# Kernel tuning notes

Measured on AMD Instinct MI355X. Metric: run time of the kernel, lower is better.

The kernel has to match this reference:

```python
import jax, jax.numpy as jnp
import numpy as np

N = 524288
H = 128
NB = 55  # number of bones


def setup_inputs() -> dict:
    key = jax.random.key(0)
    ks = jax.random.split(key, 8)
    xyz = jax.random.normal(ks[0], (N, 3), dtype=jnp.float32)
    quats = jax.random.normal(ks[1], (N, 4), dtype=jnp.float32)
    # bone transforms: identity-ish affine 4x4 per bone
    tfs = jnp.eye(4, dtype=jnp.float32)[None] + 0.05 * jax.random.normal(ks[2], (NB, 4, 4), dtype=jnp.float32)
    aabb_min = -4.0 * jnp.ones(3, dtype=jnp.float32)
    aabb_max = 4.0 * jnp.ones(3, dtype=jnp.float32)
    W0 = jax.random.normal(ks[3], (3, H), dtype=jnp.float32) / np.sqrt(3.0)
    b0 = jnp.zeros(H, dtype=jnp.float32)
    W1 = jax.random.normal(ks[4], (H, H), dtype=jnp.float32) / np.sqrt(H)
    b1 = jnp.zeros(H, dtype=jnp.float32)
    W2 = jax.random.normal(ks[5], (H, H), dtype=jnp.float32) / np.sqrt(H)
    b2 = jnp.zeros(H, dtype=jnp.float32)
    W3 = jax.random.normal(ks[6], (H, 59), dtype=jnp.float32) / np.sqrt(H)
    b3 = jnp.zeros(59, dtype=jnp.float32)
    return dict(xyz=xyz, quats=quats, tfs=tfs, aabb_min=aabb_min, aabb_max=aabb_max,
                W0=W0, b0=b0, W1=W1, b1=b1, W2=W2, b2=b2, W3=W3, b3=b3)


def hierarchical_softmax(x):
    # x: (N, 59) logits -> (N, 55) probabilities over SMPL-X bones
    s = jax.nn.sigmoid(x)

    def sm(cols):
        return jax.nn.softmax(x[:, cols], axis=-1)

    p = jnp.ones((x.shape[0], NB), x.dtype)

    def branch(p, parent, child):
        parent = np.array(parent); child = np.array(child)
        a = p[:, parent]
        p = p.at[:, child].set(a * s[:, child])
        return p.at[:, parent].set(a * (1.0 - s[:, child]))

    def subtree(p, parent, gate, children):
        children = np.array(children)
        a = p[:, parent][:, None]
        g = s[:, gate][:, None]
        p = p.at[:, children].set(a * g * sm(children))
        return p.at[:, parent].set(a[:, 0] * (1.0 - s[:, gate]))

    c123 = np.array([1, 2, 3])
    p = p.at[:, c123].set(s[:, 0:1] * sm(c123))
    p = p.at[:, 0].set(1.0 - s[:, 0])
    p = branch(p, [1, 2, 3], [4, 5, 6])
    p = branch(p, [4, 5, 6], [7, 8, 9])
    p = branch(p, [7, 8], [10, 11])
    p = subtree(p, 9, 55, [12, 13, 14])
    p = branch(p, [12], [15])
    p = branch(p, [13, 14], [16, 17])
    p = branch(p, [16, 17], [18, 19])
    p = branch(p, [18, 19], [20, 21])
    p = subtree(p, 15, 56, [22, 23, 24])
    p = subtree(p, 20, 57, [25, 28, 31, 34, 37])
    p = subtree(p, 21, 58, [40, 43, 46, 49, 52])
    p = branch(p, [25, 28, 31, 34, 37], [26, 29, 32, 35, 38])
    p = branch(p, [26, 29, 32, 35, 38], [27, 30, 33, 36, 39])
    p = branch(p, [40, 43, 46, 49, 52], [41, 44, 47, 50, 53])
    p = branch(p, [41, 44, 47, 50, 53], [42, 45, 48, 51, 54])
    return p


def build_rotation(q):
    # quaternion (w, x, y, z) -> rotation matrix, gaussian-splatting convention
    q = q / jnp.linalg.norm(q, axis=-1, keepdims=True)
    r, x, y, z = q[:, 0], q[:, 1], q[:, 2], q[:, 3]
    R = jnp.stack([
        1 - 2 * (y * y + z * z), 2 * (x * y - r * z), 2 * (x * z + r * y),
        2 * (x * y + r * z), 1 - 2 * (x * x + z * z), 2 * (y * z - r * x),
        2 * (x * z - r * y), 2 * (y * z + r * x), 1 - 2 * (x * x + y * y),
    ], axis=-1).reshape(-1, 3, 3)
    return R


def mat_to_quat(R):
    # robust matrix -> quaternion (w, x, y, z), vectorized branch selection
    m00, m01, m02 = R[:, 0, 0], R[:, 0, 1], R[:, 0, 2]
    m10, m11, m12 = R[:, 1, 0], R[:, 1, 1], R[:, 1, 2]
    m20, m21, m22 = R[:, 2, 0], R[:, 2, 1], R[:, 2, 2]
    t0 = 1 + m00 + m11 + m22
    t1 = 1 + m00 - m11 - m22
    t2 = 1 - m00 + m11 - m22
    t3 = 1 - m00 - m11 + m22
    q0 = jnp.stack([t0, m21 - m12, m02 - m20, m10 - m01], -1)
    q1 = jnp.stack([m21 - m12, t1, m01 + m10, m02 + m20], -1)
    q2 = jnp.stack([m02 - m20, m01 + m10, t2, m12 + m21], -1)
    q3 = jnp.stack([m10 - m01, m02 + m20, m12 + m21, t3], -1)
    t = jnp.stack([t0, t1, t2, t3], -1)                      # (N,4)
    qs = jnp.stack([q0, q1, q2, q3], 1)                      # (N,4,4)
    scale = 0.5 * jax.lax.rsqrt(jnp.maximum(t, 1e-8))
    qs = qs * scale[..., None]
    best = jnp.argmax(t, axis=-1)
    q = jnp.take_along_axis(qs, best[:, None, None], axis=1)[:, 0]
    return q / jnp.linalg.norm(q, axis=-1, keepdims=True)


def reference(xyz, quats, tfs, aabb_min, aabb_max, W0, b0, W1, b1, W2, b2, W3, b3):
    # aabb.normalize(xyz, sym=True)
    xyz_norm = 2.0 * (xyz - aabb_min) / (aabb_max - aabb_min) - 1.0
    # lbs_network: softplus MLP 3 -> H -> H -> H -> 59
    h = jax.nn.softplus(xyz_norm @ W0 + b0)
    h = jax.nn.softplus(h @ W1 + b1)
    h = jax.nn.softplus(h @ W2 + b2)
    logits = h @ W3 + b3                                     # (N,59)
    pts_W = hierarchical_softmax(logits)                     # (N,55)
    # blend bone transforms
    T_fwd = (pts_W @ tfs.reshape(NB, 16)).reshape(-1, 4, 4)  # (N,4,4)
    # transform points (homogeneous)
    homo = jnp.concatenate([xyz, jnp.ones((xyz.shape[0], 1), xyz.dtype)], -1)
    x_bar = jnp.einsum('nij,nj->ni', T_fwd, homo)[:, :3]
    # transform rotations
    rot_hat = build_rotation(quats)
    rot_bar = jnp.einsum('nij,njk->nik', T_fwd[:, :3, :3], rot_hat)
    quat_bar = mat_to_quat(rot_bar)
    return x_bar, rot_bar, quat_bar, T_fwd
```

## Files before the change

kernel.cpp:

```cpp
#include <hip/hip_runtime.h>
#include <hip/hip_bf16.h>
#include <math.h>

#define NPTS 524288
#define H 128
#define NB 55
#define NL 59
#define BLK 256
#define ROWB 528

typedef __attribute__((ext_vector_type(8))) short short8;
typedef __attribute__((ext_vector_type(4))) float float4v;
typedef __attribute__((ext_vector_type(2))) unsigned uint2v;

#define WS_TFHI  0
#define WS_B3P   2048
#define WS_W1HI  4096
#define WS_W1LO  36864
#define WS_W2HI  69632
#define WS_W2LO  102400
#define WS_W3HI  135168
#define WS_W3LO  151552
#define WS_TFLO  167936
#define WS_W0P   169984

#define LOG2E 1.44269504f
#define LN2   0.69314718f

__device__ __forceinline__ float fast_rcp(float x) { return __builtin_amdgcn_rcpf(x); }
__device__ __forceinline__ float fast_rsq(float x) { return __builtin_amdgcn_rsqf(x); }
__device__ __forceinline__ float sp_log2(float x) {
    return __builtin_amdgcn_logf(1.0f + __builtin_amdgcn_exp2f(x));
}
__device__ __forceinline__ float sigf(float x) {
    return fast_rcp(1.0f + __builtin_amdgcn_exp2f(-x * LOG2E));
}
__device__ __forceinline__ unsigned f2u(float f) { union { float f; unsigned u; } v; v.f = f; return v.u; }
__device__ __forceinline__ float u2f(unsigned u) { union { unsigned u; float f; } v; v.u = u; return v.f; }
__device__ __forceinline__ void split_bf(float v, short& hi, short& lo) {
    unsigned uh = (f2u(v) + 0x8000u) & 0xFFFF0000u;
    hi = (short)(uh >> 16);
    float r = v - u2f(uh);
    lo = (short)((f2u(r) + 0x8000u) >> 16);
}
__device__ __forceinline__ void pack2_hl(float a, float b, unsigned& hw, unsigned& lw) {
    unsigned ua = f2u(a) + 0x8000u, ub = f2u(b) + 0x8000u;
    hw = __builtin_amdgcn_perm(ub, ua, 0x07060302u);
    float ra = a - u2f(ua & 0xFFFF0000u);
    float rb = b - u2f(ub & 0xFFFF0000u);
    lw = __builtin_amdgcn_perm(f2u(rb) + 0x8000u, f2u(ra) + 0x8000u, 0x07060302u);
}
__device__ __forceinline__ float4v mfma16(short8 a, short8 b, float4v c) {
    return __builtin_amdgcn_mfma_f32_16x16x32_bf16(a, b, c, 0, 0, 0);
}

__global__ void prep_kernel(const float* __restrict__ W0, const float* __restrict__ W1,
                            const float* __restrict__ W2, const float* __restrict__ W3,
                            const float* __restrict__ b3, const float* __restrict__ tfs,
                            char* __restrict__ ws)
{
    const int tid = blockIdx.x * blockDim.x + threadIdx.x;
    {
        const int n = tid >> 7, k = tid & 127;
        short hi, lo;
        split_bf(W1[k * H + n], hi, lo);
        ((short*)(ws + WS_W1HI))[n * H + k] = hi;
        ((short*)(ws + WS_W1LO))[n * H + k] = lo;
        split_bf(W2[k * H + n], hi, lo);
        ((short*)(ws + WS_W2HI))[n * H + k] = hi;
        ((short*)(ws + WS_W2LO))[n * H + k] = lo;
    }
    if (tid < 64 * 128) {
        const int n = tid >> 7, k = tid & 127;
        float w = (n < NL) ? W3[k * NL + n] * LN2 : 0.0f;
        short hi, lo;
        split_bf(w, hi, lo);
        ((short*)(ws + WS_W3HI))[n * H + k] = hi;
        ((short*)(ws + WS_W3LO))[n * H + k] = lo;
    }
    if (tid < 16 * 64) {
        const int e = tid >> 6, b = tid & 63;
        float w = (b < NB) ? tfs[b * 16 + e] : 0.0f;
        short hi, lo;
        split_bf(w, hi, lo);
        ((short*)(ws + WS_TFHI))[e * 64 + b] = hi;
        ((short*)(ws + WS_TFLO))[e * 64 + b] = lo;
    }
    if (tid < 128 * 32) {
        const int n = tid >> 5, k = tid & 31;
        short s = 0;
        if (k < 9) {
            const int kk = (k < 3) ? k : ((k < 6) ? k - 3 : k - 6);
            short hi, lo;
            split_bf(W0[kk * H + n] * LOG2E, hi, lo);
            s = (k < 6) ? hi : lo;
        }
        ((short*)(ws + WS_W0P))[n * 32 + k] = s;
    }
    if (tid < 64) {
        ((float*)(ws + WS_B3P))[tid] = (tid < NL) ? b3[tid] : 0.0f;
    }
}

template<int NFT, bool SOFTPLUS>
__device__ __forceinline__ void mfma_layer(char* lds, int mrow0, int lane,
                                           const short* __restrict__ Whi,
                                           const short* __restrict__ Wlo,
                                           const float* __restrict__ bias, float bscale)
{
    const int l15 = lane & 15;
    const int g = lane >> 4;
    float4v acc[NFT][4];
#pragma unroll
    for (int ft = 0; ft < NFT; ++ft) {
        float4v bv = *(const float4v*)(bias + ft * 16 + g * 4);
        bv *= bscale;
#pragma unroll
        for (int pt = 0; pt < 4; ++pt) acc[ft][pt] = bv;
    }
#pragma unroll
    for (int k0 = 0; k0 < 128; k0 += 32) {
        short8 Bhi[4], Blo[4];
#pragma unroll
        for (int pt = 0; pt < 4; ++pt) {
            const char* rowp = lds + (mrow0 + pt * 16 + l15) * ROWB;
            Bhi[pt] = *(const short8*)(rowp + 2 * k0 + 16 * g);
            Blo[pt] = *(const short8*)(rowp + 256 + 2 * k0 + 16 * g);
        }
#pragma unroll
        for (int ft = 0; ft < NFT; ++ft) {
            short8 Ahi = *(const short8*)(Whi + (ft * 16 + l15) * H + k0 + g * 8);
            short8 Alo = *(const short8*)(Wlo + (ft * 16 + l15) * H + k0 + g * 8);
#pragma unroll
            for (int pt = 0; pt < 4; ++pt) {
                acc[ft][pt] = mfma16(Ahi, Bhi[pt], acc[ft][pt]);
                acc[ft][pt] = mfma16(Ahi, Blo[pt], acc[ft][pt]);
                acc[ft][pt] = mfma16(Alo, Bhi[pt], acc[ft][pt]);
            }
        }
    }
#pragma unroll
    for (int ft = 0; ft < NFT; ++ft) {
#pragma unroll
        for (int pt = 0; pt < 4; ++pt) {
            char* rowp = lds + (mrow0 + pt * 16 + l15) * ROWB;
            if constexpr (SOFTPLUS) {
                float s0 = sp_log2(acc[ft][pt].x);
                float s1 = sp_log2(acc[ft][pt].y);
                float s2 = sp_log2(acc[ft][pt].z);
                float s3 = sp_log2(acc[ft][pt].w);
                unsigned hx, lx, hy, ly;
                pack2_hl(s0, s1, hx, lx);
                pack2_hl(s2, s3, hy, ly);
                uint2v hw, lw;
                hw.x = hx; hw.y = hy;
                lw.x = lx; lw.y = ly;
                *(uint2v*)(rowp + (ft * 16 + g * 4) * 2) = hw;
                *(uint2v*)(rowp + 256 + (ft * 16 + g * 4) * 2) = lw;
            } else {
                *(float4v*)(rowp + (ft * 16 + g * 4) * 4) = acc[ft][pt];
            }
        }
    }
}

__global__ void __launch_bounds__(BLK, 1)
skin_kernel(const float* __restrict__ xyz, const float* __restrict__ quats,
            const float* __restrict__ amn, const float* __restrict__ amx,
            const float* __restrict__ b0, const float* __restrict__ b1,
            const float* __restrict__ b2, const char* __restrict__ ws,
            float* __restrict__ out)
{
    __shared__ __align__(16) char lds[BLK * ROWB];
    const int tid = threadIdx.x;
    const int lane = tid & 63;
    const int wv = tid >> 6;
    const int l15 = lane & 15;
    const int g = lane >> 4;
    const int mrow0 = wv * 64;
    const int n = blockIdx.x * BLK + tid;

    const float x = xyz[3 * n + 0];
    const float y = xyz[3 * n + 1];
    const float z = xyz[3 * n + 2];
    {
        const float xn = 2.0f * (x - amn[0]) * fast_rcp(amx[0] - amn[0]) - 1.0f;
        const float yn = 2.0f * (y - amn[1]) * fast_rcp(amx[1] - amn[1]) - 1.0f;
        const float zn = 2.0f * (z - amn[2]) * fast_rcp(amx[2] - amn[2]) - 1.0f;
        short xh, xl, yh, yl, zh, zl;
        split_bf(xn, xh, xl);
        split_bf(yn, yh, yl);
        split_bf(zn, zh, zl);
        short8 s0v; short8 zer = {0, 0, 0, 0, 0, 0, 0, 0};
        s0v[0] = xh; s0v[1] = yh; s0v[2] = zh; s0v[3] = xl;
        s0v[4] = yl; s0v[5] = zl; s0v[6] = xh; s0v[7] = yh;
        short8 s1v = zer; s1v[0] = zh;
        char* row = lds + tid * ROWB;
        *(short8*)(row) = s0v;
        *(short8*)(row + 16) = s1v;
        *(short8*)(row + 32) = zer;
        *(short8*)(row + 48) = zer;
    }

    {
        const short* W0p = (const short*)(ws + WS_W0P);
        float4v acc[8][4];
#pragma unroll
        for (int ft = 0; ft < 8; ++ft) {
            float4v bv = *(const float4v*)(b0 + ft * 16 + g * 4);
            bv *= LOG2E;
#pragma unroll
            for (int pt = 0; pt < 4; ++pt) acc[ft][pt] = bv;
        }
        short8 B[4];
#pragma unroll
        for (int pt = 0; pt < 4; ++pt)
            B[pt] = *(const short8*)(lds + (mrow0 + pt * 16 + l15) * ROWB + 16 * g);
#pragma unroll
        for (int ft = 0; ft < 8; ++ft) {
            short8 A = *(const short8*)(W0p + (ft * 16 + l15) * 32 + g * 8);
#pragma unroll
            for (int pt = 0; pt < 4; ++pt)
                acc[ft][pt] = mfma16(A, B[pt], acc[ft][pt]);
        }
#pragma unroll
        for (int ft = 0; ft < 8; ++ft) {
#pragma unroll
            for (int pt = 0; pt < 4; ++pt) {
                char* rowp = lds + (mrow0 + pt * 16 + l15) * ROWB;
                float s0 = sp_log2(acc[ft][pt].x);
                float s1 = sp_log2(acc[ft][pt].y);
                float s2 = sp_log2(acc[ft][pt].z);
                float s3 = sp_log2(acc[ft][pt].w);
                unsigned hx, lx, hy, ly;
                pack2_hl(s0, s1, hx, lx);
                pack2_hl(s2, s3, hy, ly);
                uint2v hw, lw;
                hw.x = hx; hw.y = hy;
                lw.x = lx; lw.y = ly;
                *(uint2v*)(rowp + (ft * 16 + g * 4) * 2) = hw;
                *(uint2v*)(rowp + 256 + (ft * 16 + g * 4) * 2) = lw;
            }
        }
    }

    mfma_layer<8, true>(lds, mrow0, lane, (const short*)(ws + WS_W1HI),
                        (const short*)(ws + WS_W1LO), b1, LOG2E);
    mfma_layer<8, true>(lds, mrow0, lane, (const short*)(ws + WS_W2HI),
                        (const short*)(ws + WS_W2LO), b2, LOG2E);
    mfma_layer<4, false>(lds, mrow0, lane, (const short*)(ws + WS_W3HI),
                         (const short*)(ws + WS_W3LO), (const float*)(ws + WS_B3P), 1.0f);

    float l[64];
#pragma unroll
    for (int j = 0; j < 16; ++j)
        *(float4v*)&l[4 * j] = *(const float4v*)(lds + tid * ROWB + 16 * j);

    float p[NB];
#define BR(par, ch)                                         \
    do {                                                    \
        float a_ = p[par];                                  \
        float s_ = sigf(l[ch]);                             \
        p[ch] = a_ * s_;                                    \
        p[par] = a_ * (1.0f - s_);                          \
    } while (0)
#define SUB3(par, gt, c0, c1, c2)                                            \
    do {                                                                     \
        float a_ = p[par];                                                   \
        float g_ = sigf(l[gt]);                                              \
        float m_ = fmaxf(l[c0], fmaxf(l[c1], l[c2]));                        \
        float e0_ = __expf(l[c0] - m_);                                      \
        float e1_ = __expf(l[c1] - m_);                                      \
        float e2_ = __expf(l[c2] - m_);                                      \
        float inv_ = a_ * g_ * fast_rcp(e0_ + e1_ + e2_);                    \
        p[c0] = e0_ * inv_;                                                  \
        p[c1] = e1_ * inv_;                                                  \
        p[c2] = e2_ * inv_;                                                  \
        p[par] = a_ * (1.0f - g_);                                           \
    } while (0)
#define SUB5(par, gt, c0, c1, c2, c3, c4)                                    \
    do {                                                                     \
        float a_ = p[par];                                                   \
        float g_ = sigf(l[gt]);                                              \
        float m_ = fmaxf(fmaxf(fmaxf(l[c0], l[c1]), fmaxf(l[c2], l[c3])), l[c4]); \
        float e0_ = __expf(l[c0] - m_);                                      \
        float e1_ = __expf(l[c1] - m_);                                      \
        float e2_ = __expf(l[c2] - m_);                                      \
        float e3_ = __expf(l[c3] - m_);                                      \
        float e4_ = __expf(l[c4] - m_);                                      \
        float inv_ = a_ * g_ * fast_rcp(e0_ + e1_ + e2_ + e3_ + e4_);        \
        p[c0] = e0_ * inv_;                                                  \
        p[c1] = e1_ * inv_;                                                  \
        p[c2] = e2_ * inv_;                                                  \
        p[c3] = e3_ * inv_;                                                  \
        p[c4] = e4_ * inv_;                                                  \
        p[par] = a_ * (1.0f - g_);                                           \
    } while (0)

    {
        float s0_ = sigf(l[0]);
        float m_ = fmaxf(l[1], fmaxf(l[2], l[3]));
        float e1_ = __expf(l[1] - m_);
        float e2_ = __expf(l[2] - m_);
        float e3_ = __expf(l[3] - m_);
        float inv_ = s0_ * fast_rcp(e1_ + e2_ + e3_);
        p[1] = e1_ * inv_;
        p[2] = e2_ * inv_;
        p[3] = e3_ * inv_;
        p[0] = 1.0f - s0_;
    }
    BR(1, 4); BR(2, 5); BR(3, 6);
    BR(4, 7); BR(5, 8); BR(6, 9);
    BR(7, 10); BR(8, 11);
    SUB3(9, 55, 12, 13, 14);
    BR(12, 15);
    BR(13, 16); BR(14, 17);
    BR(16, 18); BR(17, 19);
    BR(18, 20); BR(19, 21);
    SUB3(15, 56, 22, 23, 24);
    SUB5(20, 57, 25, 28, 31, 34, 37);
    SUB5(21, 58, 40, 43, 46, 49, 52);
    BR(25, 26); BR(28, 29); BR(31, 32); BR(34, 35); BR(37, 38);
    BR(26, 27); BR(29, 30); BR(32, 33); BR(35, 36); BR(38, 39);
    BR(40, 41); BR(43, 44); BR(46, 47); BR(49, 50); BR(52, 53);
    BR(41, 42); BR(44, 45); BR(47, 48); BR(50, 51); BR(53, 54);

    {
        char* row = lds + tid * ROWB;
#pragma unroll
        for (int jj = 0; jj < 64; jj += 4) {
            float v0 = (jj + 0 < NB) ? p[jj + 0] : 0.0f;
            float v1 = (jj + 1 < NB) ? p[jj + 1] : 0.0f;
            float v2 = (jj + 2 < NB) ? p[jj + 2] : 0.0f;
            float v3 = (jj + 3 < NB) ? p[jj + 3] : 0.0f;
            unsigned hx, lx, hy, ly;
            pack2_hl(v0, v1, hx, lx);
            pack2_hl(v2, v3, hy, ly);
            uint2v hw, lw;
            hw.x = hx; hw.y = hy;
            lw.x = lx; lw.y = ly;
            *(uint2v*)(row + 2 * jj) = hw;
            *(uint2v*)(row + 128 + 2 * jj) = lw;
        }
    }
    {
        const short* Ahi_p = (const short*)(ws + WS_TFHI);
        const short* Alo_p = (const short*)(ws + WS_TFLO);
        float4v acc[4];
#pragma unroll
        for (int pt = 0; pt < 4; ++pt) acc[pt] = (float4v){0.f, 0.f, 0.f, 0.f};
#pragma unroll
        for (int k0 = 0; k0 < 64; k0 += 32) {
            short8 Bhi[4], Blo[4];
#pragma unroll
            for (int pt = 0; pt < 4; ++pt) {
                const char* rowp = lds + (mrow0 + pt * 16 + l15) * ROWB;
                Bhi[pt] = *(const short8*)(rowp + 2 * k0 + 16 * g);
                Blo[pt] = *(const short8*)(rowp + 128 + 2 * k0 + 16 * g);
            }
            short8 Ahi = *(const short8*)(Ahi_p + l15 * 64 + k0 + g * 8);
            short8 Alo = *(const short8*)(Alo_p + l15 * 64 + k0 + g * 8);
#pragma unroll
            for (int pt = 0; pt < 4; ++pt) {
                acc[pt] = mfma16(Ahi, Bhi[pt], acc[pt]);
                acc[pt] = mfma16(Ahi, Blo[pt], acc[pt]);
                acc[pt] = mfma16(Alo, Bhi[pt], acc[pt]);
            }
        }
#pragma unroll
        for (int pt = 0; pt < 4; ++pt)
            *(float4v*)(lds + (mrow0 + pt * 16 + l15) * ROWB + 256 + g * 16) = acc[pt];
    }
    float T[16];
#pragma unroll
    for (int j = 0; j < 4; ++j)
        *(float4v*)&T[4 * j] = *(const float4v*)(lds + tid * ROWB + 256 + 16 * j);

    const float xb0 = fmaf(T[0], x, fmaf(T[1], y, fmaf(T[2], z, T[3])));
    const float xb1 = fmaf(T[4], x, fmaf(T[5], y, fmaf(T[6], z, T[7])));
    const float xb2 = fmaf(T[8], x, fmaf(T[9], y, fmaf(T[10], z, T[11])));

    float qr = quats[4 * n + 0];
    float qx = quats[4 * n + 1];
    float qy = quats[4 * n + 2];
    float qz = quats[4 * n + 3];
    {
        float inv = fast_rsq(qr * qr + qx * qx + qy * qy + qz * qz);
        qr *= inv; qx *= inv; qy *= inv; qz *= inv;
    }
    const float R00 = 1.0f - 2.0f * (qy * qy + qz * qz);
    const float R01 = 2.0f * (qx * qy - qr * qz);
    const float R02 = 2.0f * (qx * qz + qr * qy);
    const float R10 = 2.0f * (qx * qy + qr * qz);
    const float R11 = 1.0f - 2.0f * (qx * qx + qz * qz);
    const float R12 = 2.0f * (qy * qz - qr * qx);
    const float R20 = 2.0f * (qx * qz - qr * qy);
    const float R21 = 2.0f * (qy * qz + qr * qx);
    const float R22 = 1.0f - 2.0f * (qx * qx + qy * qy);

    const float B00 = T[0] * R00 + T[1] * R10 + T[2] * R20;
    const float B01 = T[0] * R01 + T[1] * R11 + T[2] * R21;
    const float B02 = T[0] * R02 + T[1] * R12 + T[2] * R22;
    const float B10 = T[4] * R00 + T[5] * R10 + T[6] * R20;
    const float B11 = T[4] * R01 + T[5] * R11 + T[6] * R21;
    const float B12 = T[4] * R02 + T[5] * R12 + T[6] * R22;
    const float B20 = T[8] * R00 + T[9] * R10 + T[10] * R20;
    const float B21 = T[8] * R01 + T[9] * R11 + T[10] * R21;
    const float B22 = T[8] * R02 + T[9] * R12 + T[10] * R22;

    const float t0 = 1.0f + B00 + B11 + B22;
    const float t1 = 1.0f + B00 - B11 - B22;
    const float t2 = 1.0f - B00 + B11 - B22;
    const float t3 = 1.0f - B00 - B11 + B22;
    const float s0 = 0.5f * fast_rsq(fmaxf(t0, 1e-8f));
    const float s1 = 0.5f * fast_rsq(fmaxf(t1, 1e-8f));
    const float s2 = 0.5f * fast_rsq(fmaxf(t2, 1e-8f));
    const float s3 = 0.5f * fast_rsq(fmaxf(t3, 1e-8f));
    const float q0w = t0 * s0, q0x = (B21 - B12) * s0, q0y = (B02 - B20) * s0, q0z = (B10 - B01) * s0;
    const float q1w = (B21 - B12) * s1, q1x = t1 * s1, q1y = (B01 + B10) * s1, q1z = (B02 + B20) * s1;
    const float q2w = (B02 - B20) * s2, q2x = (B01 + B10) * s2, q2y = t2 * s2, q2z = (B12 + B21) * s2;
    const float q3w = (B10 - B01) * s3, q3x = (B02 + B20) * s3, q3y = (B12 + B21) * s3, q3z = t3 * s3;

    int best = 0;
    float tb = t0;
    if (t1 > tb) { best = 1; tb = t1; }
    if (t2 > tb) { best = 2; tb = t2; }
    if (t3 > tb) { best = 3; tb = t3; }

    float Qw = (best == 0) ? q0w : (best == 1) ? q1w : (best == 2) ? q2w : q3w;
    float Qx = (best == 0) ? q0x : (best == 1) ? q1x : (best == 2) ? q2x : q3x;
    float Qy = (best == 0) ? q0y : (best == 1) ? q1y : (best == 2) ? q2y : q3y;
    float Qz = (best == 0) ? q0z : (best == 1) ? q1z : (best == 2) ? q2z : q3z;
    {
        float inv = fast_rsq(Qw * Qw + Qx * Qx + Qy * Qy + Qz * Qz);
        Qw *= inv; Qx *= inv; Qy *= inv; Qz *= inv;
    }

    out[3 * n + 0] = xb0;
    out[3 * n + 1] = xb1;
    out[3 * n + 2] = xb2;
    float* rb = out + 3 * (size_t)NPTS;
    rb[9 * n + 0] = B00; rb[9 * n + 1] = B01; rb[9 * n + 2] = B02;
    rb[9 * n + 3] = B10; rb[9 * n + 4] = B11; rb[9 * n + 5] = B12;
    rb[9 * n + 6] = B20; rb[9 * n + 7] = B21; rb[9 * n + 8] = B22;
    float4* qb = (float4*)(out + 12 * (size_t)NPTS);
    qb[n] = make_float4(Qw, Qx, Qy, Qz);
    float4* tf = (float4*)(out + 16 * (size_t)NPTS);
    tf[4 * n + 0] = make_float4(T[0], T[1], T[2], T[3]);
    tf[4 * n + 1] = make_float4(T[4], T[5], T[6], T[7]);
    tf[4 * n + 2] = make_float4(T[8], T[9], T[10], T[11]);
    tf[4 * n + 3] = make_float4(T[12], T[13], T[14], T[15]);
}

extern "C" void kernel_launch(void* const* d_in, const int* in_sizes, int n_in,
                              void* d_out, int out_size, void* d_ws, size_t ws_size,
                              hipStream_t stream) {
    const float* xyz = (const float*)d_in[0];
    const float* quats = (const float*)d_in[1];
    const float* tfs = (const float*)d_in[2];
    const float* amn = (const float*)d_in[3];
    const float* amx = (const float*)d_in[4];
    const float* W0 = (const float*)d_in[5];
    const float* b0 = (const float*)d_in[6];
    const float* W1 = (const float*)d_in[7];
    const float* b1 = (const float*)d_in[8];
    const float* W2 = (const float*)d_in[9];
    const float* b2 = (const float*)d_in[10];
    const float* W3 = (const float*)d_in[11];
    const float* b3 = (const float*)d_in[12];
    float* out = (float*)d_out;
    char* ws = (char*)d_ws;

    hipLaunchKernelGGL(prep_kernel, dim3(64), dim3(256), 0, stream, W0, W1, W2, W3, b3, tfs, ws);
    hipLaunchKernelGGL(skin_kernel, dim3(NPTS / BLK), dim3(BLK), 0, stream,
                       xyz, quats, amn, amx, b0, b1, b2, (const char*)ws, out);
}
```

Baseline: 332.0 us.

## Stash low-bf16 activation halves in registers to halve LDS rows and double occupancy

The low-precision halves of each hidden activation now stay in registers instead of a second LDS region, so the per-row LDS stride drops from 528 to 272 bytes. Each MFMA layer becomes two passes. The first runs the hi×hi and lo-weight×hi products, then the stashed low halves are written over the same row slot for a second pass with hi weights. This shrinks the block's LDS footprint so two blocks can share a CU, and launch bounds are raised to 2 to match. The cost is 64 extra live VGPRs per thread on top of large accumulators, which risks spills under the tighter register budget.

```diff
diff --git a/kernel.cpp b/kernel.cpp
--- a/kernel.cpp
+++ b/kernel.cpp
@@ -7,7 +7,7 @@
 #define NB 55
 #define NL 59
 #define BLK 256
-#define ROWB 528
+#define ROWB 272
 
 typedef __attribute__((ext_vector_type(8))) short short8;
 typedef __attribute__((ext_vector_type(4))) float float4v;
@@ -106,7 +106,8 @@
 __device__ __forceinline__ void mfma_layer(char* lds, int mrow0, int lane,
                                            const short* __restrict__ Whi,
                                            const short* __restrict__ Wlo,
-                                           const float* __restrict__ bias, float bscale)
+                                           const float* __restrict__ bias, float bscale,
+                                           uint2v (&stash)[8][4])
 {
     const int l15 = lane & 15;
     const int g = lane >> 4;
@@ -120,12 +121,11 @@
     }
 #pragma unroll
     for (int k0 = 0; k0 < 128; k0 += 32) {
-        short8 Bhi[4], Blo[4];
+        short8 Bhi[4];
 #pragma unroll
         for (int pt = 0; pt < 4; ++pt) {
             const char* rowp = lds + (mrow0 + pt * 16 + l15) * ROWB;
             Bhi[pt] = *(const short8*)(rowp + 2 * k0 + 16 * g);
-            Blo[pt] = *(const short8*)(rowp + 256 + 2 * k0 + 16 * g);
         }
 #pragma unroll
         for (int ft = 0; ft < NFT; ++ft) {
@@ -134,9 +134,32 @@
 #pragma unroll
             for (int pt = 0; pt < 4; ++pt) {
                 acc[ft][pt] = mfma16(Ahi, Bhi[pt], acc[ft][pt]);
-                acc[ft][pt] = mfma16(Ahi, Blo[pt], acc[ft][pt]);
                 acc[ft][pt] = mfma16(Alo, Bhi[pt], acc[ft][pt]);
             }
+        }
+    }
+#pragma unroll
+    for (int ft = 0; ft < 8; ++ft) {
+#pragma unroll
+        for (int pt = 0; pt < 4; ++pt) {
+            char* rowp = lds + (mrow0 + pt * 16 + l15) * ROWB;
+            *(uint2v*)(rowp + (ft * 16 + g * 4) * 2) = stash[ft][pt];
+        }
+    }
+#pragma unroll
+    for (int k0 = 0; k0 < 128; k0 += 32) {
+        short8 Blo[4];
+#pragma unroll
+        for (int pt = 0; pt < 4; ++pt) {
+            const char* rowp = lds + (mrow0 + pt * 16 + l15) * ROWB;
+            Blo[pt] = *(const short8*)(rowp + 2 * k0 + 16 * g);
+        }
+#pragma unroll
+        for (int ft = 0; ft < NFT; ++ft) {
+            short8 Ahi = *(const short8*)(Whi + (ft * 16 + l15) * H + k0 + g * 8);
+#pragma unroll
+            for (int pt = 0; pt < 4; ++pt)
+                acc[ft][pt] = mfma16(Ahi, Blo[pt], acc[ft][pt]);
         }
     }
 #pragma unroll
@@ -156,7 +179,7 @@
                 hw.x = hx; hw.y = hy;
                 lw.x = lx; lw.y = ly;
                 *(uint2v*)(rowp + (ft * 16 + g * 4) * 2) = hw;
-                *(uint2v*)(rowp + 256 + (ft * 16 + g * 4) * 2) = lw;
+                stash[ft][pt] = lw;
             } else {
                 *(float4v*)(rowp + (ft * 16 + g * 4) * 4) = acc[ft][pt];
             }
@@ -164,7 +187,7 @@
     }
 }
 
-__global__ void __launch_bounds__(BLK, 1)
+__global__ void __launch_bounds__(BLK, 2)
 skin_kernel(const float* __restrict__ xyz, const float* __restrict__ quats,
             const float* __restrict__ amn, const float* __restrict__ amx,
             const float* __restrict__ b0, const float* __restrict__ b1,
@@ -179,6 +202,8 @@
     const int g = lane >> 4;
     const int mrow0 = wv * 64;
     const int n = blockIdx.x * BLK + tid;
+
+    uint2v stash[8][4];
 
     const float x = xyz[3 * n + 0];
     const float y = xyz[3 * n + 1];
@@ -239,17 +264,17 @@
                 hw.x = hx; hw.y = hy;
                 lw.x = lx; lw.y = ly;
                 *(uint2v*)(rowp + (ft * 16 + g * 4) * 2) = hw;
-                *(uint2v*)(rowp + 256 + (ft * 16 + g * 4) * 2) = lw;
+                stash[ft][pt] = lw;
             }
         }
     }
 
     mfma_layer<8, true>(lds, mrow0, lane, (const short*)(ws + WS_W1HI),
-                        (const short*)(ws + WS_W1LO), b1, LOG2E);
+                        (const short*)(ws + WS_W1LO), b1, LOG2E, stash);
     mfma_layer<8, true>(lds, mrow0, lane, (const short*)(ws + WS_W2HI),
-                        (const short*)(ws + WS_W2LO), b2, LOG2E);
+                        (const short*)(ws + WS_W2LO), b2, LOG2E, stash);
     mfma_layer<4, false>(lds, mrow0, lane, (const short*)(ws + WS_W3HI),
-                         (const short*)(ws + WS_W3LO), (const float*)(ws + WS_B3P), 1.0f);
+                         (const short*)(ws + WS_W3LO), (const float*)(ws + WS_B3P), 1.0f, stash);
 
     float l[64];
 #pragma unroll
@@ -369,12 +394,12 @@
         }
 #pragma unroll
         for (int pt = 0; pt < 4; ++pt)
-            *(float4v*)(lds + (mrow0 + pt * 16 + l15) * ROWB + 256 + g * 16) = acc[pt];
+            *(float4v*)(lds + (mrow0 + pt * 16 + l15) * ROWB + g * 16) = acc[pt];
     }
     float T[16];
 #pragma unroll
     for (int j = 0; j < 4; ++j)
-        *(float4v*)&T[4 * j] = *(const float4v*)(lds + tid * ROWB + 256 + 16 * j);
+        *(float4v*)&T[4 * j] = *(const float4v*)(lds + tid * ROWB + 16 * j);
 
     const float xb0 = fmaf(T[0], x, fmaf(T[1], y, fmaf(T[2], z, T[3])));
     const float xb1 = fmaf(T[4], x, fmaf(T[5], y, fmaf(T[6], z, T[7])));
```

New measurement: 471.0 us. 1.42x slower.
